# Optimization experiments

Measured on AMD Instinct MI355X. Metric: run time of the kernel, lower is better.

The kernel has to match this reference:

```python
import jax, jax.numpy as jnp
import numpy as np

NEG_SLOPE = 0.01  # torch F.leaky_relu default
BN_EPS = 1e-5
N_GRAPHS = 256


def _bn(x, gamma, beta):
    # training-mode BatchNorm1d per head over the node axis; x: [N, H, O]
    mu = x.mean(axis=0)
    var = x.var(axis=0)
    return (x - mu) * jax.lax.rsqrt(var + BN_EPS) * gamma + beta


def _gat_layer(h, src, dst, snorm, fcW, aS, aD, gamma, beta):
    # h: [N, Din]; fcW: [H, Din, O]; aS/aD/gamma/beta: [H, O]
    N = h.shape[0]
    z = jnp.einsum('nd,hdo->nho', h, fcW)                 # [N, H, O]
    el = jnp.einsum('nho,ho->nh', z, aS)                  # attn_fc src half
    er = jnp.einsum('nho,ho->nh', z, aD)                  # attn_fc dst half
    e = jax.nn.leaky_relu(el[src] + er[dst], NEG_SLOPE)   # [E, H]
    emax = jax.ops.segment_max(e, dst, num_segments=N)    # softmax over in-edges
    ee = jnp.exp(e - emax[dst])
    denom = jax.ops.segment_sum(ee, dst, num_segments=N)
    alpha = ee / denom[dst]                               # [E, H]
    msg = alpha[:, :, None] * z[src]                      # [E, H, O]
    agg = jax.ops.segment_sum(msg, dst, num_segments=N)   # [N, H, O]
    agg = agg * snorm[:, None, None]                      # graph_norm
    agg = _bn(agg, gamma, beta)                           # batch_norm
    out = jax.nn.elu(agg).reshape(N, -1)                  # concat heads
    return h + out                                        # residual (Din == H*O)


def setup_inputs() -> dict:
    key = jax.random.key(0)
    ks = jax.random.split(key, 32)
    N, E, G = 50000, 1600000, N_GRAPHS
    DIN, H, O, D, NC = 128, 8, 16, 128, 10
    L_mid = 3  # L-1 multi-head layers

    graph_ids = jnp.sort(jax.random.randint(ks[0], (N,), 0, G))
    counts = jax.ops.segment_sum(jnp.ones((N,), jnp.float32), graph_ids, num_segments=G)
    snorm = (1.0 / jnp.sqrt(jnp.maximum(counts, 1.0)))[graph_ids]  # nodes_num_norm_sqrt
    src = jax.random.randint(ks[1], (E,), 0, N)
    dst = jax.random.randint(ks[2], (E,), 0, N)

    def nrm(k, shape, s=0.1):
        return jax.random.normal(k, shape, jnp.float32) * s

    return {
        'nodes_feat': jax.random.normal(ks[3], (N, DIN), jnp.float32),
        'snorm': snorm,
        'emb_W': nrm(ks[4], (DIN, D)), 'emb_b': jnp.zeros((D,), jnp.float32),
        'fcW': nrm(ks[5], (L_mid, H, D, O)),
        'aS': nrm(ks[6], (L_mid, H, O)), 'aD': nrm(ks[7], (L_mid, H, O)),
        'gamma': jnp.ones((L_mid, H, O), jnp.float32),
        'beta': jnp.zeros((L_mid, H, O), jnp.float32),
        'fcW_last': nrm(ks[8], (1, D, D)),
        'aS_last': nrm(ks[9], (1, D)), 'aD_last': nrm(ks[10], (1, D)),
        'g_last': jnp.ones((1, D), jnp.float32), 'b_last': jnp.zeros((1, D), jnp.float32),
        'w1': nrm(ks[11], (D, D // 2)), 'b1': jnp.zeros((D // 2,), jnp.float32),
        'w2': nrm(ks[12], (D // 2, D // 4)), 'b2': jnp.zeros((D // 4,), jnp.float32),
        'w3': nrm(ks[13], (D // 4, NC)), 'b3': jnp.zeros((NC,), jnp.float32),
        'src': src, 'dst': dst, 'graph_ids': graph_ids,
    }


def reference(nodes_feat, snorm, emb_W, emb_b, fcW, aS, aD, gamma, beta,
              fcW_last, aS_last, aD_last, g_last, b_last,
              w1, b1, w2, b2, w3, b3, src, dst, graph_ids):
    h = nodes_feat @ emb_W + emb_b                        # embedding_h
    for l in range(fcW.shape[0]):                         # L-1 multi-head GAT layers
        h = _gat_layer(h, src, dst, snorm, fcW[l], aS[l], aD[l], gamma[l], beta[l])
    h = _gat_layer(h, src, dst, snorm, fcW_last, aS_last, aD_last, g_last, b_last)
    # mean_nodes readout over variable-size graphs
    counts = jax.ops.segment_sum(jnp.ones_like(snorm), graph_ids, num_segments=N_GRAPHS)
    hg = jax.ops.segment_sum(h, graph_ids, num_segments=N_GRAPHS)
    hg = hg / jnp.maximum(counts, 1.0)[:, None]           # [G, D]
    # MLPReadout: D -> D/2 -> D/4 -> n_classes
    y = jax.nn.relu(hg @ w1 + b1)
    y = jax.nn.relu(y @ w2 + b2)
    return y @ w3 + b3
```

## Files before the change

kernel.cpp:

```cpp
#include <hip/hip_runtime.h>
#include <hip/hip_bf16.h>
#include <hip/hip_fp16.h>

typedef __hip_bfloat16 bf16;
typedef __attribute__((ext_vector_type(8))) short short8;
typedef __attribute__((ext_vector_type(4))) float floatx4;

__device__ __forceinline__ float ldc(const void* p, size_t i, int code) {
    if (code == 1) return __bfloat162float(((const bf16*)p)[i]);
    if (code == 2) return __half2float(((const __half*)p)[i]);
    return ((const float*)p)[i];
}
__device__ __forceinline__ void stc(void* p, size_t i, int code, float v) {
    if (code == 1) ((bf16*)p)[i] = __float2bfloat16(v);
    else if (code == 2) ((__half*)p)[i] = __float2half(v);
    else ((float*)p)[i] = v;
}
__device__ __forceinline__ unsigned int pk2(float a, float b) {
    unsigned int ua = __float_as_uint(a); ua += 0x7fffu + ((ua >> 16) & 1u);
    unsigned int ub = __float_as_uint(b); ub += 0x7fffu + ((ub >> 16) & 1u);
    return (ua >> 16) | (ub & 0xffff0000u);
}

__global__ void k_detect(const unsigned short* __restrict__ g, int* __restrict__ code) {
    unsigned short a = g[0], b = g[1], c = g[2], d = g[3];
    int r;
    if (a == 0x3F80 && b == 0x3F80 && c == 0x3F80 && d == 0x3F80) r = 1;
    else if (a == 0x3C00 && b == 0x3C00 && c == 0x3C00 && d == 0x3C00) r = 2;
    else r = 3;
    *code = r;
}

__global__ void k_zero_i(int* p, int n) { int i = blockIdx.x * 256 + threadIdx.x; if (i < n) p[i] = 0; }
__global__ void k_zero_f(float* p, int n) { int i = blockIdx.x * 256 + threadIdx.x; if (i < n) p[i] = 0.f; }
__global__ void k_sent(void* o, int n, float v, const int* codep) {
    int code = *codep;
    int i = blockIdx.x * 256 + threadIdx.x;
    if (i < n) stc(o, i, code, v);
}

struct CvtArgs { const void* src[17]; int off[18]; };
__global__ void k_cvt_all(float* __restrict__ dst, CvtArgs a,
                          const int* __restrict__ codep, int total) {
    int i = blockIdx.x * 256 + threadIdx.x;
    if (i >= total) return;
    int code = *codep;
    int seg = 0;
    #pragma unroll
    for (int k = 0; k < 16; ++k) seg += (i >= a.off[k + 1]) ? 1 : 0;
    dst[i] = ldc(a.src[seg], i - a.off[seg], code);
}

#define ETILE 8192
__global__ __launch_bounds__(256) void k_bcount(const int* __restrict__ dst,
        int* __restrict__ bcnt, int E, int nbuck) {
    __shared__ int h[200];
    int t = threadIdx.x;
    for (int i = t; i < nbuck; i += 256) h[i] = 0;
    __syncthreads();
    int e0 = blockIdx.x * ETILE;
    int n = min(ETILE, E - e0);
    for (int i = t; i < n; i += 256) atomicAdd(&h[dst[e0 + i] >> 8], 1);
    __syncthreads();
    for (int i = t; i < nbuck; i += 256)
        if (h[i]) atomicAdd(&bcnt[i], h[i]);
}

__global__ void k_scan(const int* __restrict__ cnt, int* __restrict__ off,
                       int* __restrict__ cur, int n) {
    __shared__ int sums[1024];
    int tid = threadIdx.x;
    int C = (n + 1023) >> 10;
    int lo = tid * C, hi = min(lo + C, n);
    int s = 0;
    for (int i = lo; i < hi; ++i) s += cnt[i];
    sums[tid] = s;
    __syncthreads();
    for (int o = 1; o < 1024; o <<= 1) {
        int v = (tid >= o) ? sums[tid - o] : 0;
        __syncthreads();
        sums[tid] += v;
        __syncthreads();
    }
    int run = (tid > 0) ? sums[tid - 1] : 0;
    for (int i = lo; i < hi; ++i) { off[i] = run; cur[i] = run; run += cnt[i]; }
    if (tid == 1023) off[n] = sums[1023];
}

__global__ __launch_bounds__(256) void k_bscat(const int* __restrict__ src,
        const int* __restrict__ dst, int* __restrict__ bcur,
        unsigned int* __restrict__ ebuf, int E, int nbuck) {
    __shared__ unsigned int eord[ETILE];
    __shared__ int cnt[200], lst[200], cur[200], gb[200];
    int t = threadIdx.x;
    int e0 = blockIdx.x * ETILE;
    int n = min(ETILE, E - e0);
    for (int i = t; i < nbuck; i += 256) cnt[i] = 0;
    __syncthreads();
    for (int i = t; i < n; i += 256) atomicAdd(&cnt[dst[e0 + i] >> 8], 1);
    __syncthreads();
    if (t == 0) {
        int run = 0;
        for (int b = 0; b < nbuck; ++b) { int c = cnt[b]; lst[b] = run; cur[b] = run; run += c; }
    }
    __syncthreads();
    for (int b = t; b < nbuck; b += 256)
        gb[b] = cnt[b] ? atomicAdd(&bcur[b], cnt[b]) : 0;
    for (int i = t; i < n; i += 256) {
        int d = dst[e0 + i];
        int pos = atomicAdd(&cur[d >> 8], 1);
        eord[pos] = ((unsigned int)d << 16) | (unsigned int)src[e0 + i];
    }
    __syncthreads();
    for (int i = t; i < n; i += 256) {
        unsigned int pk = eord[i];
        int b = pk >> 24;
        ebuf[gb[b] + (i - lst[b])] = pk;
    }
}

__global__ __launch_bounds__(256) void k_fscatter(const unsigned int* __restrict__ ebuf,
        const int* __restrict__ boff, int* __restrict__ row_off,
        unsigned short* __restrict__ col_src, int N, int E) {
    __shared__ int cnt[256], cur[256];
    int b = blockIdx.x, t = threadIdx.x;
    int lo = boff[b], hi = boff[b + 1];
    int nodelo = b << 8;
    cnt[t] = 0;
    __syncthreads();
    for (int j = lo + t; j < hi; j += 256)
        atomicAdd(&cnt[(int)(ebuf[j] >> 16) - nodelo], 1);
    __syncthreads();
    if (t == 0) {
        int run = lo;
        for (int i = 0; i < 256; ++i) { int c = cnt[i]; cur[i] = run; cnt[i] = run; run += c; }
    }
    __syncthreads();
    int node = nodelo + t;
    if (node < N) row_off[node] = cnt[t];
    if (t == 0 && b == (int)gridDim.x - 1) row_off[N] = E;
    for (int j = lo + t; j < hi; j += 256) {
        unsigned int pk = ebuf[j];
        int pos = atomicAdd(&cur[(int)(pk >> 16) - nodelo], 1);
        col_src[pos] = (unsigned short)(pk & 0xffffu);
    }
}

#define WB_STRIDE 136
#define WB_MAT 19584
__global__ void k_wtrans(const void* __restrict__ fcW, const void* __restrict__ fcW_last,
                         const void* __restrict__ emb_W,
                         const float* __restrict__ aSf, const float* __restrict__ aDf,
                         const float* __restrict__ aSlf, const float* __restrict__ aDlf,
                         unsigned short* __restrict__ Wb, const int* __restrict__ codep) {
    int code = *codep;
    int idx = blockIdx.x * 256 + threadIdx.x;
    if (idx >= 5 * WB_MAT) return;
    int m = idx / WB_MAT, rem = idx % WB_MAT;
    int c = rem / WB_STRIDE, k = rem % WB_STRIDE;
    float v = 0.f;
    if (k < 128) {
        if (m == 0) {
            if (c < 128) v = ldc(emb_W, k * 128 + c, code);
        } else if (m <= 3) {
            int l = m - 1;
            if (c < 128) v = ldc(fcW, l * 16384 + (c >> 4) * 2048 + k * 16 + (c & 15), code);
            else if (c < 136) {
                int hh = c - 128; float s = 0.f;
                for (int o = 0; o < 16; ++o)
                    s += ldc(fcW, l * 16384 + hh * 2048 + k * 16 + o, code) * aSf[l * 128 + hh * 16 + o];
                v = s;
            } else {
                int hh = c - 136; float s = 0.f;
                for (int o = 0; o < 16; ++o)
                    s += ldc(fcW, l * 16384 + hh * 2048 + k * 16 + o, code) * aDf[l * 128 + hh * 16 + o];
                v = s;
            }
        } else {
            if (c < 128) v = ldc(fcW_last, k * 128 + c, code);
            else if (c == 128) { float s = 0.f; for (int o = 0; o < 128; ++o) s += ldc(fcW_last, k * 128 + o, code) * aSlf[o]; v = s; }
            else if (c == 129) { float s = 0.f; for (int o = 0; o < 128; ++o) s += ldc(fcW_last, k * 128 + o, code) * aDlf[o]; v = s; }
        }
    }
    Wb[idx] = (unsigned short)(pk2(v, 0.f) & 0xffffu);
}

__global__ __launch_bounds__(256) void k_gemm(const void* __restrict__ Av, int a_raw,
        const int* __restrict__ codep, const unsigned short* __restrict__ Wbm,
        const float* __restrict__ bias, float* __restrict__ outf,
        unsigned int* __restrict__ zb,
        float* __restrict__ el, float* __restrict__ er, int H, int N) {
    __shared__ unsigned short Wl[WB_MAT];
    int tid = threadIdx.x;
    {
        const uint4* s4 = (const uint4*)Wbm;
        uint4* d4 = (uint4*)Wl;
        for (int i = tid; i < WB_MAT / 8; i += 256) d4[i] = s4[i];
    }
    int wave = tid >> 6, lane = tid & 63;
    int c15 = lane & 15, quad = lane >> 4;
    int rowb = blockIdx.x * 64 + wave * 16;
    int myrow = rowb + c15;
    bool rowok = myrow < N;
    int code = a_raw ? *codep : 3;

    floatx4 acc[9];
    #pragma unroll
    for (int i = 0; i < 9; ++i) acc[i] = (floatx4){0.f, 0.f, 0.f, 0.f};

    __syncthreads();
    #pragma unroll
    for (int ks = 0; ks < 4; ++ks) {
        int k0 = ks * 32 + quad * 8;
        short8 a;
        if (!rowok) {
            a = (short8){0, 0, 0, 0, 0, 0, 0, 0};
        } else if (code == 1) {
            union { uint4 u; short8 s; } cv;
            cv.u = *(const uint4*)((const unsigned short*)Av + (size_t)myrow * 128 + k0);
            a = cv.s;
        } else if (code == 3) {
            const float* ap = (const float*)Av + (size_t)myrow * 128 + k0;
            float4 x = *(const float4*)ap;
            float4 y = *(const float4*)(ap + 4);
            union { uint4 u; short8 s; } cv;
            cv.u = make_uint4(pk2(x.x, x.y), pk2(x.z, x.w), pk2(y.x, y.y), pk2(y.z, y.w));
            a = cv.s;
        } else {
            const __half* ap = (const __half*)Av + (size_t)myrow * 128 + k0;
            union { uint4 u; short8 s; } cv;
            cv.u = make_uint4(pk2(__half2float(ap[0]), __half2float(ap[1])),
                              pk2(__half2float(ap[2]), __half2float(ap[3])),
                              pk2(__half2float(ap[4]), __half2float(ap[5])),
                              pk2(__half2float(ap[6]), __half2float(ap[7])));
            a = cv.s;
        }
        #pragma unroll
        for (int ct = 0; ct < 9; ++ct) {
            union { uint4 u; short8 s; } bv;
            bv.u = *(const uint4*)&Wl[(ct * 16 + c15) * WB_STRIDE + k0];
            acc[ct] = __builtin_amdgcn_mfma_f32_16x16x32_bf16(a, bv.s, acc[ct], 0, 0, 0);
        }
    }

    if (zb == nullptr) {
        #pragma unroll
        for (int ct = 0; ct < 8; ++ct) {
            int c = ct * 16 + c15;
            float bj = bias ? bias[c] : 0.f;
            #pragma unroll
            for (int r = 0; r < 4; ++r) {
                int n = rowb + quad * 4 + r;
                if (n < N) outf[(size_t)n * 128 + c] = acc[ct][r] + bj;
            }
        }
    } else {
        #pragma unroll
        for (int ct = 0; ct < 8; ++ct) {
            #pragma unroll
            for (int r = 0; r < 4; ++r) {
                float v = acc[ct][r];
                float vx = __shfl_xor(v, 1);
                if ((c15 & 1) == 0) {
                    int n = rowb + quad * 4 + r;
                    if (n < N) zb[(size_t)n * 64 + ct * 8 + (c15 >> 1)] = pk2(v, vx);
                }
            }
        }
        #pragma unroll
        for (int r = 0; r < 4; ++r) {
            int n = rowb + quad * 4 + r;
            if (n < N) {
                float v = acc[8][r];
                if (c15 < H) el[n * H + c15] = v;
                else if (c15 < 2 * H) er[n * H + (c15 - H)] = v;
            }
        }
    }
}

__global__ __launch_bounds__(256) void k_agg(const unsigned int* __restrict__ zb,
        const float* __restrict__ el, const float* __restrict__ er,
        const int* __restrict__ row_off, const unsigned short* __restrict__ col_src,
        const float* __restrict__ snormf, float* __restrict__ agg,
        int N, int H) {
    int n = blockIdx.x * 4 + (threadIdx.x >> 6);
    if (n >= N) return;
    int lane = threadIdx.x & 63;
    int half = lane >> 5;
    int sub = lane & 31;
    int hha = (H == 8) ? (sub >> 2) : 0;
    int wh  = (H == 8) ? (lane >> 3) : 0;
    float er_t = er[n * H + hha];
    float er_w = er[n * H + wh];
    int beg = row_off[n], end = row_off[n + 1];
    float l = 0.f, c0 = 0.f, c1 = 0.f, c2 = 0.f, c3 = 0.f;
    int nb = (end - beg) >> 3;
    int j = beg;
    if (nb > 0) {
        int sv = col_src[beg + (lane & 7)];
        float ew = el[sv * H + wh] + er_w;
        int s0 = __shfl(sv, half, 8);
        int s1 = __shfl(sv, 2 + half, 8);
        int s2 = __shfl(sv, 4 + half, 8);
        int s3 = __shfl(sv, 6 + half, 8);
        uint2 v0 = *(const uint2*)(zb + (size_t)s0 * 64 + sub * 2);
        uint2 v1 = *(const uint2*)(zb + (size_t)s1 * 64 + sub * 2);
        uint2 v2 = *(const uint2*)(zb + (size_t)s2 * 64 + sub * 2);
        uint2 v3 = *(const uint2*)(zb + (size_t)s3 * 64 + sub * 2);
        for (int b = 0; b < nb; ++b) {
            int jn = j + 8;
            int sv_n = 0; float ew_n = 0.f;
            uint2 n0 = make_uint2(0, 0), n1 = n0, n2 = n0, n3 = n0;
            if (b + 1 < nb) {
                sv_n = col_src[jn + (lane & 7)];
                ew_n = el[sv_n * H + wh] + er_w;
                int t0 = __shfl(sv_n, half, 8);
                int t1 = __shfl(sv_n, 2 + half, 8);
                int t2 = __shfl(sv_n, 4 + half, 8);
                int t3 = __shfl(sv_n, 6 + half, 8);
                n0 = *(const uint2*)(zb + (size_t)t0 * 64 + sub * 2);
                n1 = *(const uint2*)(zb + (size_t)t1 * 64 + sub * 2);
                n2 = *(const uint2*)(zb + (size_t)t2 * 64 + sub * 2);
                n3 = *(const uint2*)(zb + (size_t)t3 * 64 + sub * 2);
            }
            float e = (ew > 0.f) ? ew : 0.01f * ew;
            float w = __expf(fminf(e, 60.f));
            int wb_ = hha << 3;
            float w0 = __shfl(w, wb_ + half);
            float w1 = __shfl(w, wb_ + 2 + half);
            float w2 = __shfl(w, wb_ + 4 + half);
            float w3 = __shfl(w, wb_ + 6 + half);
            l += (w0 + w1) + (w2 + w3);
            c0 = fmaf(w0, __uint_as_float(v0.x << 16), c0);
            c1 = fmaf(w0, __uint_as_float(v0.x & 0xffff0000u), c1);
            c2 = fmaf(w0, __uint_as_float(v0.y << 16), c2);
            c3 = fmaf(w0, __uint_as_float(v0.y & 0xffff0000u), c3);
            c0 = fmaf(w1, __uint_as_float(v1.x << 16), c0);
            c1 = fmaf(w1, __uint_as_float(v1.x & 0xffff0000u), c1);
            c2 = fmaf(w1, __uint_as_float(v1.y << 16), c2);
            c3 = fmaf(w1, __uint_as_float(v1.y & 0xffff0000u), c3);
            c0 = fmaf(w2, __uint_as_float(v2.x << 16), c0);
            c1 = fmaf(w2, __uint_as_float(v2.x & 0xffff0000u), c1);
            c2 = fmaf(w2, __uint_as_float(v2.y << 16), c2);
            c3 = fmaf(w2, __uint_as_float(v2.y & 0xffff0000u), c3);
            c0 = fmaf(w3, __uint_as_float(v3.x << 16), c0);
            c1 = fmaf(w3, __uint_as_float(v3.x & 0xffff0000u), c1);
            c2 = fmaf(w3, __uint_as_float(v3.y << 16), c2);
            c3 = fmaf(w3, __uint_as_float(v3.y & 0xffff0000u), c3);
            sv = sv_n; ew = ew_n;
            v0 = n0; v1 = n1; v2 = n2; v3 = n3;
            j = jn;
        }
    }
    for (; j < end; j += 2) {
        int idx = j + half;
        bool act = idx < end;
        int si = col_src[act ? idx : j];
        float e = el[si * H + hha] + er_t;
        e = (e > 0.f) ? e : 0.01f * e;
        float w = act ? __expf(fminf(e, 60.f)) : 0.f;
        uint2 v = *(const uint2*)(zb + (size_t)si * 64 + sub * 2);
        l += w;
        c0 = fmaf(w, __uint_as_float(v.x << 16), c0);
        c1 = fmaf(w, __uint_as_float(v.x & 0xffff0000u), c1);
        c2 = fmaf(w, __uint_as_float(v.y << 16), c2);
        c3 = fmaf(w, __uint_as_float(v.y & 0xffff0000u), c3);
    }
    l  += __shfl_xor(l, 32);
    c0 += __shfl_xor(c0, 32);
    c1 += __shfl_xor(c1, 32);
    c2 += __shfl_xor(c2, 32);
    c3 += __shfl_xor(c3, 32);
    if (half == 0) {
        float sn = snormf[n];
        float inv = (end > beg) ? sn / l : 0.f;
        float4 o = make_float4(c0 * inv, c1 * inv, c2 * inv, c3 * inv);
        *(float4*)&agg[(size_t)n * 128 + 4 * sub] = o;
    }
}

#define BN_BLOCKS 256
__global__ void k_bnstats1(const float* __restrict__ agg, float* __restrict__ pstats, int N) {
    int c = threadIdx.x;
    float s = 0.f, q = 0.f;
    for (int n = blockIdx.x; n < N; n += gridDim.x) {
        float v = agg[(size_t)n * 128 + c];
        s += v; q += v * v;
    }
    pstats[blockIdx.x * 256 + c] = s;
    pstats[blockIdx.x * 256 + 128 + c] = q;
}
__global__ void k_bnstats2(const float* __restrict__ pstats, float* __restrict__ stats,
                           const float* __restrict__ gamma, const float* __restrict__ beta,
                           int nb, float invN) {
    int c = threadIdx.x;
    float s0 = 0.f, s1 = 0.f, q0 = 0.f, q1 = 0.f;
    int b = 0;
    for (; b + 1 < nb; b += 2) {
        s0 += pstats[b * 256 + c];
        q0 += pstats[b * 256 + 128 + c];
        s1 += pstats[(b + 1) * 256 + c];
        q1 += pstats[(b + 1) * 256 + 128 + c];
    }
    for (; b < nb; ++b) { s0 += pstats[b * 256 + c]; q0 += pstats[b * 256 + 128 + c]; }
    float s = s0 + s1, q = q0 + q1;
    float mu = s * invN;
    float var = fmaxf(q * invN - mu * mu, 0.f);
    float A = rsqrtf(var + 1e-5f) * gamma[c];
    stats[c] = A;
    stats[128 + c] = fmaf(-mu, A, beta[c]);
}
__global__ void k_bnapply(const float* __restrict__ agg, const float* __restrict__ stats,
        float* __restrict__ h, int N) {
    int idx = blockIdx.x * 256 + threadIdx.x;
    if (idx >= N * 128) return;
    int c = idx & 127;
    float xn = fmaf(agg[idx], stats[c], stats[128 + c]);
    float y = (xn > 0.f) ? xn : (__expf(xn) - 1.0f);
    h[idx] += y;
}

__global__ void k_gsum(const float* __restrict__ h, const int* __restrict__ gids,
                       float* __restrict__ hg, float* __restrict__ gcnt, int N) {
    int c = threadIdx.x;
    int base = blockIdx.x * 64;
    int endi = min(base + 64, N);
    int gprev = -1; float acc = 0.f; int cnt = 0;
    for (int n = base; n < endi; ++n) {
        int g = gids[n];
        if (g != gprev) {
            if (gprev >= 0) {
                atomicAdd(&hg[gprev * 128 + c], acc);
                if (c == 0) atomicAdd(&gcnt[gprev], (float)cnt);
            }
            gprev = g; acc = 0.f; cnt = 0;
        }
        acc += h[(size_t)n * 128 + c];
        ++cnt;
    }
    if (gprev >= 0) {
        atomicAdd(&hg[gprev * 128 + c], acc);
        if (c == 0) atomicAdd(&gcnt[gprev], (float)cnt);
    }
}
__global__ void k_mlp(const float* __restrict__ hg, const float* __restrict__ gcnt,
        const float* __restrict__ w1, const float* __restrict__ b1,
        const float* __restrict__ w2, const float* __restrict__ b2,
        const float* __restrict__ w3, const float* __restrict__ b3,
        void* __restrict__ out, const int* __restrict__ codep) {
    __shared__ float xs[128], y1[64], y2[32];
    int g = blockIdx.x, tid = threadIdx.x;
    float inv = 1.0f / fmaxf(gcnt[g], 1.0f);
    xs[tid]      = hg[g * 128 + tid] * inv;
    xs[tid + 64] = hg[g * 128 + 64 + tid] * inv;
    __syncthreads();
    float a = b1[tid];
    for (int k = 0; k < 128; ++k) a = fmaf(xs[k], w1[k * 64 + tid], a);
    y1[tid] = fmaxf(a, 0.f);
    __syncthreads();
    if (tid < 32) {
        float a2 = b2[tid];
        for (int k = 0; k < 64; ++k) a2 = fmaf(y1[k], w2[k * 32 + tid], a2);
        y2[tid] = fmaxf(a2, 0.f);
    }
    __syncthreads();
    if (tid < 10) {
        float a3 = b3[tid];
        for (int k = 0; k < 32; ++k) a3 = fmaf(y2[k], w3[k * 10 + tid], a3);
        stc(out, g * 10 + tid, *codep, a3);
    }
}

extern "C" void kernel_launch(void* const* d_in, const int* in_sizes, int n_in,
                              void* d_out, int out_size, void* d_ws, size_t ws_size,
                              hipStream_t stream) {
    const void* nodes_feat = d_in[0];
    const void* snorm      = d_in[1];
    const void* emb_W      = d_in[2];
    const void* fcW        = d_in[4];
    const void* gamma      = d_in[7];
    const void* fcW_last   = d_in[9];
    const int*  src        = (const int*)d_in[20];
    const int*  dst        = (const int*)d_in[21];
    const int*  gids       = (const int*)d_in[22];

    const int N = 50000, E = 1600000, G = 256;
    const int NBUCK = (N + 255) >> 8;
    const int NTILE = (E + ETILE - 1) / ETILE;
    const int PTOT = 29226 + N;

    char* p = (char*)d_ws;
    auto alloc = [&](size_t bytes) { char* r = p; p += (bytes + 255) & ~(size_t)255; return r; };
    int*   code    = (int*)alloc(256);
    float* h       = (float*)alloc((size_t)N * 128 * 4);
    unsigned int* zb = (unsigned int*)alloc((size_t)N * 64 * 4);
    float* agg     = (float*)alloc((size_t)N * 128 * 4);
    float* el      = (float*)alloc((size_t)N * 8 * 4);
    float* er      = (float*)alloc((size_t)N * 8 * 4);
    int*   bcnt    = (int*)alloc((size_t)NBUCK * 4);
    int*   boff    = (int*)alloc((size_t)(NBUCK + 1) * 4);
    int*   bcur    = (int*)alloc((size_t)NBUCK * 4);
    unsigned int* ebuf = (unsigned int*)alloc((size_t)E * 4);
    int*   row_off = (int*)alloc((size_t)(N + 1) * 4);
    unsigned short* col_src = (unsigned short*)alloc((size_t)E * 2);
    unsigned short* Wb = (unsigned short*)alloc((size_t)5 * WB_MAT * 2);
    float* pstats  = (float*)alloc((size_t)BN_BLOCKS * 256 * 4);
    float* stats   = (float*)alloc(256 * 4);
    float* hg      = (float*)alloc((size_t)G * 128 * 4 + (size_t)G * 4);
    float* gcnt    = hg + (size_t)G * 128;
    float* params  = (float*)alloc((size_t)PTOT * 4);

    const int OFF[18] = {0, 16384, 16512, 16896, 17280, 17664, 18048, 18176,
                         18304, 18432, 18560, 26752, 26816, 28864, 28896, 29216, 29226, PTOT};
    float* emb_bf = params + OFF[1];
    float* aSf    = params + OFF[2];
    float* aDf    = params + OFF[3];
    float* gf     = params + OFF[4];
    float* bf     = params + OFF[5];
    float* aSlf   = params + OFF[6];
    float* aDlf   = params + OFF[7];
    float* glf    = params + OFF[8];
    float* blf    = params + OFF[9];
    float* w1f    = params + OFF[10];
    float* b1f    = params + OFF[11];
    float* w2f    = params + OFF[12];
    float* b2f_   = params + OFF[13];
    float* w3f    = params + OFF[14];
    float* b3f    = params + OFF[15];
    float* snormf = params + OFF[16];

    k_detect<<<1, 1, 0, stream>>>((const unsigned short*)gamma, code);

    bool ok = (n_in == 23) && (out_size == G * 10) &&
              (in_sizes[0] == N * 128) && (in_sizes[1] == N) &&
              (in_sizes[4] == 3 * 8 * 128 * 16) && (in_sizes[7] == 384) &&
              (in_sizes[9] == 16384) &&
              (in_sizes[20] == E) && (in_sizes[21] == E) && (in_sizes[22] == N);
    size_t need = (size_t)(p - (char*)d_ws);
    if (!ok || ws_size < need) {
        k_sent<<<(out_size + 255) / 256, 256, 0, stream>>>(d_out, out_size, ok ? 123.0f : 150.0f, code);
        return;
    }

    CvtArgs ca;
    const int srcidx[17] = {2, 3, 5, 6, 7, 8, 10, 11, 12, 13, 14, 15, 16, 17, 18, 19, 1};
    for (int k = 0; k < 17; ++k) ca.src[k] = d_in[srcidx[k]];
    for (int k = 0; k < 18; ++k) ca.off[k] = OFF[k];
    k_cvt_all<<<(PTOT + 255) / 256, 256, 0, stream>>>(params, ca, code, PTOT);
    k_wtrans<<<(5 * WB_MAT + 255) / 256, 256, 0, stream>>>(
        fcW, fcW_last, emb_W, aSf, aDf, aSlf, aDlf, Wb, code);

    k_zero_i<<<1, 256, 0, stream>>>(bcnt, NBUCK);
    k_bcount<<<NTILE, 256, 0, stream>>>(dst, bcnt, E, NBUCK);
    k_scan<<<1, 1024, 0, stream>>>(bcnt, boff, bcur, NBUCK);
    k_bscat<<<NTILE, 256, 0, stream>>>(src, dst, bcur, ebuf, E, NBUCK);
    k_fscatter<<<NBUCK, 256, 0, stream>>>(ebuf, boff, row_off, col_src, N, E);

    int gblk = (N + 63) / 64;
    k_gemm<<<gblk, 256, 0, stream>>>(nodes_feat, 1, code, Wb, emb_bf, h,
                                     nullptr, nullptr, nullptr, 0, N);

    for (int l = 0; l < 4; ++l) {
        const unsigned short* Wl_ = Wb + (size_t)(l + 1) * WB_MAT;
        const float *gl, *bl; int H;
        if (l < 3) { gl = gf + l * 128; bl = bf + l * 128; H = 8; }
        else       { gl = glf;          bl = blf;          H = 1; }
        k_gemm<<<gblk, 256, 0, stream>>>(h, 0, code, Wl_, nullptr, nullptr,
                                         zb, el, er, H, N);
        k_agg<<<(N + 3) / 4, 256, 0, stream>>>(zb, el, er, row_off, col_src, snormf,
                                               agg, N, H);
        k_bnstats1<<<BN_BLOCKS, 128, 0, stream>>>(agg, pstats, N);
        k_bnstats2<<<1, 128, 0, stream>>>(pstats, stats, gl, bl, BN_BLOCKS, 1.0f / (float)N);
        k_bnapply<<<(N * 128 + 255) / 256, 256, 0, stream>>>(agg, stats, h, N);
    }

    k_zero_f<<<(G * 129 + 255) / 256, 256, 0, stream>>>(hg, G * 129);
    k_gsum<<<(N + 63) / 64, 128, 0, stream>>>(h, gids, hg, gcnt, N);
    k_mlp<<<G, 64, 0, stream>>>(hg, gcnt, w1f, b1f, w2f, b2f_, w3f, b3f, d_out, code);
}
```

Measured before the change: 960.1 us.

## Fuse BatchNorm apply, ELU and residual into next GEMM load and readout

Removes the separate BN-apply kernel. Each following GEMM now normalises agg, applies ELU, adds the residual while loading its A operand, and writes the updated h back. The final layer's apply is folded into the graph-sum readout. BN stats pass 1 also moves to 256 threads with a shared-memory reduction, and stats pass 2 is unrolled. This saves one full read-modify-write pass over h per layer, at the cost of extra loads and an exp inside the GEMM prologue.

```diff
diff --git a/kernel.cpp b/kernel.cpp
--- a/kernel.cpp
+++ b/kernel.cpp
@@ -189,13 +189,17 @@
         const int* __restrict__ codep, const unsigned short* __restrict__ Wbm,
         const float* __restrict__ bias, float* __restrict__ outf,
         unsigned int* __restrict__ zb,
-        float* __restrict__ el, float* __restrict__ er, int H, int N) {
+        float* __restrict__ el, float* __restrict__ er, int H, int N,
+        const float* __restrict__ aggp, const float* __restrict__ bnAB,
+        float* __restrict__ hres) {
     __shared__ unsigned short Wl[WB_MAT];
+    __shared__ float sAB[256];
     int tid = threadIdx.x;
     {
         const uint4* s4 = (const uint4*)Wbm;
         uint4* d4 = (uint4*)Wl;
         for (int i = tid; i < WB_MAT / 8; i += 256) d4[i] = s4[i];
+        if (aggp) sAB[tid] = bnAB[tid];
     }
     int wave = tid >> 6, lane = tid & 63;
     int c15 = lane & 15, quad = lane >> 4;
@@ -215,6 +219,26 @@
         short8 a;
         if (!rowok) {
             a = (short8){0, 0, 0, 0, 0, 0, 0, 0};
+        } else if (aggp) {
+            const float* hp = (const float*)Av + (size_t)myrow * 128 + k0;
+            const float* ap = aggp + (size_t)myrow * 128 + k0;
+            float hv[8], av[8], yv[8];
+            *(float4*)hv = *(const float4*)hp; *(float4*)(hv + 4) = *(const float4*)(hp + 4);
+            *(float4*)av = *(const float4*)ap; *(float4*)(av + 4) = *(const float4*)(ap + 4);
+            #pragma unroll
+            for (int i = 0; i < 8; ++i) {
+                int c = k0 + i;
+                float xn = fmaf(av[i], sAB[c], sAB[128 + c]);
+                float e = (xn > 0.f) ? xn : (__expf(xn) - 1.f);
+                yv[i] = hv[i] + e;
+            }
+            float* op = hres + (size_t)myrow * 128 + k0;
+            *(float4*)op = *(float4*)yv;
+            *(float4*)(op + 4) = *(float4*)(yv + 4);
+            union { uint4 u; short8 s; } cv;
+            cv.u = make_uint4(pk2(yv[0], yv[1]), pk2(yv[2], yv[3]),
+                              pk2(yv[4], yv[5]), pk2(yv[6], yv[7]));
+            a = cv.s;
         } else if (code == 1) {
             union { uint4 u; short8 s; } cv;
             cv.u = *(const uint4*)((const unsigned short*)Av + (size_t)myrow * 128 + k0);
@@ -381,49 +405,56 @@
 }
 
 #define BN_BLOCKS 256
-__global__ void k_bnstats1(const float* __restrict__ agg, float* __restrict__ pstats, int N) {
-    int c = threadIdx.x;
+__global__ __launch_bounds__(256) void k_bnstats1(const float* __restrict__ agg,
+        float* __restrict__ pstats, int N) {
+    __shared__ float red[256];
+    int t = threadIdx.x;
+    int c = t & 127, hfl = t >> 7;
     float s = 0.f, q = 0.f;
-    for (int n = blockIdx.x; n < N; n += gridDim.x) {
+    for (int n = blockIdx.x * 2 + hfl; n < N; n += 512) {
         float v = agg[(size_t)n * 128 + c];
         s += v; q += v * v;
     }
-    pstats[blockIdx.x * 256 + c] = s;
-    pstats[blockIdx.x * 256 + 128 + c] = q;
+    red[t] = s;
+    __syncthreads();
+    if (hfl == 0) s += red[128 + c];
+    __syncthreads();
+    red[t] = q;
+    __syncthreads();
+    if (hfl == 0) {
+        q += red[128 + c];
+        pstats[blockIdx.x * 256 + c] = s;
+        pstats[blockIdx.x * 256 + 128 + c] = q;
+    }
 }
 __global__ void k_bnstats2(const float* __restrict__ pstats, float* __restrict__ stats,
                            const float* __restrict__ gamma, const float* __restrict__ beta,
                            int nb, float invN) {
     int c = threadIdx.x;
-    float s0 = 0.f, s1 = 0.f, q0 = 0.f, q1 = 0.f;
+    float sA[4] = {0.f, 0.f, 0.f, 0.f}, qA[4] = {0.f, 0.f, 0.f, 0.f};
     int b = 0;
-    for (; b + 1 < nb; b += 2) {
-        s0 += pstats[b * 256 + c];
-        q0 += pstats[b * 256 + 128 + c];
-        s1 += pstats[(b + 1) * 256 + c];
-        q1 += pstats[(b + 1) * 256 + 128 + c];
-    }
-    for (; b < nb; ++b) { s0 += pstats[b * 256 + c]; q0 += pstats[b * 256 + 128 + c]; }
-    float s = s0 + s1, q = q0 + q1;
+    for (; b + 3 < nb; b += 4) {
+        #pragma unroll
+        for (int u = 0; u < 4; ++u) {
+            sA[u] += pstats[(b + u) * 256 + c];
+            qA[u] += pstats[(b + u) * 256 + 128 + c];
+        }
+    }
+    for (; b < nb; ++b) { sA[0] += pstats[b * 256 + c]; qA[0] += pstats[b * 256 + 128 + c]; }
+    float s = (sA[0] + sA[1]) + (sA[2] + sA[3]);
+    float q = (qA[0] + qA[1]) + (qA[2] + qA[3]);
     float mu = s * invN;
     float var = fmaxf(q * invN - mu * mu, 0.f);
     float A = rsqrtf(var + 1e-5f) * gamma[c];
     stats[c] = A;
     stats[128 + c] = fmaf(-mu, A, beta[c]);
 }
-__global__ void k_bnapply(const float* __restrict__ agg, const float* __restrict__ stats,
-        float* __restrict__ h, int N) {
-    int idx = blockIdx.x * 256 + threadIdx.x;
-    if (idx >= N * 128) return;
-    int c = idx & 127;
-    float xn = fmaf(agg[idx], stats[c], stats[128 + c]);
-    float y = (xn > 0.f) ? xn : (__expf(xn) - 1.0f);
-    h[idx] += y;
-}
-
-__global__ void k_gsum(const float* __restrict__ h, const int* __restrict__ gids,
+
+__global__ void k_gsum(const float* __restrict__ h, const float* __restrict__ aggp,
+                       const float* __restrict__ stats, const int* __restrict__ gids,
                        float* __restrict__ hg, float* __restrict__ gcnt, int N) {
     int c = threadIdx.x;
+    float A = stats[c], B = stats[128 + c];
     int base = blockIdx.x * 64;
     int endi = min(base + 64, N);
     int gprev = -1; float acc = 0.f; int cnt = 0;
@@ -436,7 +467,10 @@
             }
             gprev = g; acc = 0.f; cnt = 0;
         }
-        acc += h[(size_t)n * 128 + c];
+        size_t idx = (size_t)n * 128 + c;
+        float xn = fmaf(aggp[idx], A, B);
+        float e = (xn > 0.f) ? xn : (__expf(xn) - 1.f);
+        acc += h[idx] + e;
         ++cnt;
     }
     if (gprev >= 0) {
@@ -559,7 +593,8 @@
 
     int gblk = (N + 63) / 64;
     k_gemm<<<gblk, 256, 0, stream>>>(nodes_feat, 1, code, Wb, emb_bf, h,
-                                     nullptr, nullptr, nullptr, 0, N);
+                                     nullptr, nullptr, nullptr, 0, N,
+                                     nullptr, nullptr, nullptr);
 
     for (int l = 0; l < 4; ++l) {
         const unsigned short* Wl_ = Wb + (size_t)(l + 1) * WB_MAT;
@@ -567,15 +602,17 @@
         if (l < 3) { gl = gf + l * 128; bl = bf + l * 128; H = 8; }
         else       { gl = glf;          bl = blf;          H = 1; }
         k_gemm<<<gblk, 256, 0, stream>>>(h, 0, code, Wl_, nullptr, nullptr,
-                                         zb, el, er, H, N);
+                                         zb, el, er, H, N,
+                                         (l > 0) ? agg : nullptr,
+                                         (l > 0) ? stats : nullptr,
+                                         (l > 0) ? h : nullptr);
         k_agg<<<(N + 3) / 4, 256, 0, stream>>>(zb, el, er, row_off, col_src, snormf,
                                                agg, N, H);
-        k_bnstats1<<<BN_BLOCKS, 128, 0, stream>>>(agg, pstats, N);
+        k_bnstats1<<<BN_BLOCKS, 256, 0, stream>>>(agg, pstats, N);
         k_bnstats2<<<1, 128, 0, stream>>>(pstats, stats, gl, bl, BN_BLOCKS, 1.0f / (float)N);
-        k_bnapply<<<(N * 128 + 255) / 256, 256, 0, stream>>>(agg, stats, h, N);
     }
 
     k_zero_f<<<(G * 129 + 255) / 256, 256, 0, stream>>>(hg, G * 129);
-    k_gsum<<<(N + 63) / 64, 128, 0, stream>>>(h, gids, hg, gcnt, N);
+    k_gsum<<<(N + 63) / 64, 128, 0, stream>>>(h, agg, stats, gids, hg, gcnt, N);
     k_mlp<<<G, 64, 0, stream>>>(hg, gcnt, w1f, b1f, w2f, b2f_, w3f, b3f, d_out, code);
 }
```

After: 777.0 us. 1.24x faster.
